# Optimization experiments

Hardware: AMD Instinct MI355X
Metric: run time of the kernel (lower is better)

Reference implementation:

```python
import jax, jax.numpy as jnp
import numpy as np

NUM_HEADS = 16


def setup_inputs() -> dict:
    key = jax.random.key(0)
    ks = jax.random.split(key, 10)
    B, T, D = 2, 2048, 1024
    s = D ** -0.5  # keep activations O(1)
    return {
        "inputs": jax.random.normal(ks[0], (B, T, D), dtype=jnp.float32),
        "mask": jax.random.randint(ks[1], (B, T, T), 0, 2, dtype=jnp.int32),
        "Wq": jax.random.normal(ks[2], (D, D), dtype=jnp.float32) * s,
        "bq": jnp.zeros((D,), dtype=jnp.float32),
        "Wk": jax.random.normal(ks[3], (D, D), dtype=jnp.float32) * s,
        "bk": jnp.zeros((D,), dtype=jnp.float32),
        "Wv": jax.random.normal(ks[4], (D, D), dtype=jnp.float32) * s,
        "bv": jnp.zeros((D,), dtype=jnp.float32),
        "Wo": jax.random.normal(ks[5], (D, D), dtype=jnp.float32) * s,
        "bo": jnp.zeros((D,), dtype=jnp.float32),
    }


def _split_heads(x, h):
    # [B,T,D] -> [B,H,T,D/H]
    B, T, D = x.shape
    return x.reshape(B, T, h, D // h).transpose(0, 2, 1, 3)


def reference(inputs, mask, Wq, bq, Wk, bk, Wv, bv, Wo, bo):
    B, T, D = inputs.shape
    H = NUM_HEADS
    dh = D // H
    q = _split_heads(inputs @ Wq + bq, H) * (dh ** -0.5)  # [B,H,T,dh]
    k = _split_heads(inputs @ Wk + bk, H)
    v = _split_heads(inputs @ Wv + bv, H)
    dot = jnp.einsum("bhqd,bhkd->bhqk", q, k)  # [B,H,T,T]
    m = mask.astype(jnp.float32)[:, None]  # [B,1,T,T]
    dot = dot * m + (1.0 - m) * jnp.finfo(jnp.float32).min
    attn = jax.nn.softmax(dot, axis=-1)
    # dropout inactive at inference (training=False)
    heads = jnp.einsum("bhqk,bhkd->bhqd", attn, v)
    combined = heads.transpose(0, 2, 1, 3).reshape(B, T, D)
    return combined @ Wo + bo
```

## Files before the change

kernel.cpp:

```cpp
#include <hip/hip_runtime.h>
#include <hip/hip_bf16.h>
#include <stdint.h>

typedef _Float16 f16;
typedef __attribute__((ext_vector_type(8))) _Float16 f16x8;
typedef __attribute__((ext_vector_type(2))) __fp16 fp16x2;
typedef __attribute__((ext_vector_type(4))) float f32x4;
typedef __attribute__((ext_vector_type(16))) float f32x16;

#define B_  2
#define T_  2048
#define D_  1024
#define H_  16
#define DH_ 64
#define NSPLIT 2
#define KVSPAN (T_ / NSPLIT)

__device__ __forceinline__ f32x4 mfma16f(f16x8 a, f16x8 b, f32x4 c) {
    return __builtin_amdgcn_mfma_f32_16x16x32_f16(a, b, c, 0, 0, 0);
}
__device__ __forceinline__ f32x16 mfma32f(f16x8 a, f16x8 b, f32x16 c) {
    return __builtin_amdgcn_mfma_f32_32x32x16_f16(a, b, c, 0, 0, 0);
}
__device__ __forceinline__ void gload16(const void* g, void* l) {
    __builtin_amdgcn_global_load_lds(
        (const __attribute__((address_space(1))) uint32_t*)g,
        (__attribute__((address_space(3))) uint32_t*)l, 16, 0, 0);
}
__device__ __forceinline__ float xmax32(float x) {
    float a, b;
    asm("v_mov_b32 %0, %2\n\t"
        "v_mov_b32 %1, %2\n\t"
        "s_nop 1\n\t"
        "v_permlane32_swap_b32 %0, %1\n\t"
        "s_nop 1\n\t"
        "v_max_f32 %0, %0, %1"
        : "=&v"(a), "=&v"(b) : "v"(x));
    return a;
}
__device__ __forceinline__ float xsum32(float x) {
    float a, b;
    asm("v_mov_b32 %0, %2\n\t"
        "v_mov_b32 %1, %2\n\t"
        "s_nop 1\n\t"
        "v_permlane32_swap_b32 %0, %1\n\t"
        "s_nop 1\n\t"
        "v_add_f32 %0, %0, %1"
        : "=&v"(a), "=&v"(b) : "v"(x));
    return a;
}

__global__ __launch_bounds__(256) void maskpack_kernel(
    const int* __restrict__ mask, uint32_t* __restrict__ bitsT)
{
    size_t e = (size_t)blockIdx.x * 256 + threadIdx.x;
    unsigned long long bb = __ballot(mask[e] != 0);
    if ((threadIdx.x & 63) == 0) {
        size_t r = e >> 11;
        int b = (int)(r >> 11), q = (int)(r & (T_ - 1));
        int k = (int)(e & (T_ - 1));
        int w0 = k >> 5;
        size_t base = (size_t)b * (64 * T_) + q;
        bitsT[base + (size_t)w0 * T_]       = (uint32_t)bb;
        bitsT[base + (size_t)(w0 + 1) * T_] = (uint32_t)(bb >> 32);
    }
}

__global__ __launch_bounds__(256) void cvtx_kernel(
    const float* __restrict__ X, f16* __restrict__ Xh)
{
    size_t i0 = ((size_t)blockIdx.x * 256 + threadIdx.x) * 8;
    float4 a = *(const float4*)(X + i0);
    float4 b = *(const float4*)(X + i0 + 4);
    float v[8] = {a.x, a.y, a.z, a.w, b.x, b.y, b.z, b.w};
    f16x8 hh;
#pragma unroll
    for (int i = 0; i < 8; ++i) hh[i] = (f16)v[i];
    *(f16x8*)(Xh + i0) = hh;
}

__global__ __launch_bounds__(256) void wtr_kernel(
    const float* __restrict__ Wq, const float* __restrict__ Wk,
    const float* __restrict__ Wv, const float* __restrict__ Wo,
    f16* __restrict__ WqT, f16* __restrict__ WkT,
    f16* __restrict__ WvT, f16* __restrict__ WoT)
{
    __shared__ float s_t[64][65];
    const int zz = blockIdx.z;
    const float* __restrict__ W = (zz == 0) ? Wq : (zz == 1) ? Wk : (zz == 2) ? Wv : Wo;
    const int k0 = blockIdx.y * 64, n0 = blockIdx.x * 64;
    const int t = threadIdx.x;
    const int r = t >> 2, c0 = (t & 3) * 16;

#pragma unroll
    for (int j = 0; j < 4; ++j) {
        float4 v = *(const float4*)(W + (size_t)(k0 + r) * D_ + n0 + c0 + j * 4);
        s_t[r][c0 + j * 4 + 0] = v.x;
        s_t[r][c0 + j * 4 + 1] = v.y;
        s_t[r][c0 + j * 4 + 2] = v.z;
        s_t[r][c0 + j * 4 + 3] = v.w;
    }
    __syncthreads();

    const int n = t >> 2, kc = (t & 3) * 16;
    f16x8 h0, h1;
#pragma unroll
    for (int j = 0; j < 8; ++j) h0[j] = (f16)s_t[kc + j][n];
#pragma unroll
    for (int j = 0; j < 8; ++j) h1[j] = (f16)s_t[kc + 8 + j][n];
    f16* dh = (zz == 0) ? WqT : (zz == 1) ? WkT : (zz == 2) ? WvT : WoT;
    size_t o = (size_t)(n0 + n) * D_ + k0 + kc;
    *(f16x8*)(dh + o) = h0;
    *(f16x8*)(dh + o + 8) = h1;
}

__global__ __launch_bounds__(256) void gemm_kernel(
    const f16* __restrict__ A, int zbase,
    const f16* __restrict__ BqT, const f16* __restrict__ BkT,
    const f16* __restrict__ BvT, const f16* __restrict__ BoT,
    const float* __restrict__ bq, const float* __restrict__ bk,
    const float* __restrict__ bv, const float* __restrict__ bo,
    f16* __restrict__ Q, f16* __restrict__ K,
    f16* __restrict__ Vt, float* __restrict__ outF)
{
    __shared__ f16 sA[128 * 32];
    __shared__ f16 sB[128 * 32];

    const int z = blockIdx.z + zbase;
    const f16* __restrict__ Bm = (z == 0) ? BqT : (z == 1) ? BkT : (z == 2) ? BvT : BoT;
    const float* __restrict__ bias = (z == 0) ? bq : (z == 1) ? bk : (z == 2) ? bv : bo;

    const int m0 = blockIdx.y * 128;
    const int n0 = blockIdx.x * 128;
    const int tid = threadIdx.x;
    const int w = tid >> 6, l = tid & 63;
    const int g = l >> 4, lr = l & 15;
    const int wm = w >> 1, wn = w & 1;

    const int srow = w * 32 + (l >> 2);
    const int skb  = (l & 3) * 8;

    f32x4 acc[4][4] = {};

    for (int k0 = 0; k0 < D_; k0 += 32) {
        __syncthreads();
#pragma unroll
        for (int i = 0; i < 2; ++i) {
            gload16(A  + (size_t)(m0 + srow + i * 16) * D_ + k0 + skb,
                    &sA[w * 1024 + i * 512]);
            gload16(Bm + (size_t)(n0 + srow + i * 16) * D_ + k0 + skb,
                    &sB[w * 1024 + i * 512]);
        }
        __syncthreads();

        f16x8 ah[4], bh[4];
#pragma unroll
        for (int f = 0; f < 4; ++f) {
            ah[f] = *(const f16x8*)&sA[(wm * 64 + f * 16 + lr) * 32 + g * 8];
            bh[f] = *(const f16x8*)&sB[(wn * 64 + f * 16 + lr) * 32 + g * 8];
        }
#pragma unroll
        for (int fm = 0; fm < 4; ++fm)
#pragma unroll
            for (int fn = 0; fn < 4; ++fn)
                acc[fm][fn] = mfma16f(ah[fm], bh[fn], acc[fm][fn]);
    }

    const float scale = (z == 0) ? 0.125f : 1.0f;
    float biasv[4];
#pragma unroll
    for (int f = 0; f < 4; ++f) biasv[f] = bias[n0 + wn * 64 + f * 16 + lr];

    if (z <= 1) {
        f16* Oq = (z == 0) ? Q : K;
#pragma unroll
        for (int fm = 0; fm < 4; ++fm)
#pragma unroll
            for (int fn = 0; fn < 4; ++fn)
#pragma unroll
                for (int j = 0; j < 4; ++j) {
                    int r = m0 + wm * 64 + fm * 16 + g * 4 + j;
                    int c = n0 + wn * 64 + fn * 16 + lr;
                    float v = (acc[fm][fn][j] + biasv[fn]) * scale;
                    int b = r >> 11, t = r & (T_ - 1);
                    int h = (c >> 6) & 15, d = c & 63;
                    Oq[((size_t)(b * H_ + h) * T_ + t) * DH_ + d] = (f16)v;
                }
    } else if (z == 2) {
#pragma unroll
        for (int fm = 0; fm < 4; ++fm)
#pragma unroll
            for (int fn = 0; fn < 4; ++fn) {
                int r0 = m0 + wm * 64 + fm * 16 + g * 4;
                int c  = n0 + wn * 64 + fn * 16 + lr;
                int b = r0 >> 11, t0 = r0 & (T_ - 1);
                int h = (c >> 6) & 15, d = c & 63;
                union { f16 h4[4]; uint2 u; } pk;
#pragma unroll
                for (int j = 0; j < 4; ++j)
                    pk.h4[j] = (f16)(acc[fm][fn][j] + biasv[fn]);
                *(uint2*)&Vt[(size_t)(b * H_ + h) * (T_ * DH_) +
                             (size_t)(t0 >> 5) * (32 * DH_) + d * 32 + (t0 & 31)] = pk.u;
            }
    } else {
#pragma unroll
        for (int fm = 0; fm < 4; ++fm)
#pragma unroll
            for (int fn = 0; fn < 4; ++fn)
#pragma unroll
                for (int j = 0; j < 4; ++j) {
                    int r = m0 + wm * 64 + fm * 16 + g * 4 + j;
                    int c = n0 + wn * 64 + fn * 16 + lr;
                    outF[(size_t)r * D_ + c] = acc[fm][fn][j] + biasv[fn];
                }
    }
}

__device__ __forceinline__ void attn_tile(
    const f16x8* kh, const f16x8* vb, uint32_t mw, const f16x8* qf,
    f32x16& o0, f32x16& o1, float& m_run, float& l_run)
{
    const float L2E = 1.4426950408889634f;
    f32x16 s = {};
    __builtin_amdgcn_s_setprio(1);
    s = mfma32f(kh[0], qf[0], s);
    s = mfma32f(kh[1], qf[1], s);
    s = mfma32f(kh[2], qf[2], s);
    s = mfma32f(kh[3], qf[3], s);
    __builtin_amdgcn_s_setprio(0);

#pragma unroll
    for (int r = 0; r < 16; ++r) {
        const int bit = (r & 3) + 8 * (r >> 2);
        if (!((mw >> bit) & 1u)) s[r] = -1e30f;
    }

    float t8[8], t4[4];
#pragma unroll
    for (int i = 0; i < 8; ++i) t8[i] = fmaxf(s[i], s[i + 8]);
#pragma unroll
    for (int i = 0; i < 4; ++i) t4[i] = fmaxf(t8[i], t8[i + 4]);
    float pm = fmaxf(fmaxf(t4[0], t4[2]), fmaxf(t4[1], t4[3]));
    pm = xmax32(pm);

    if (__any(pm > m_run + 8.0f)) {
        float mn  = fmaxf(m_run, pm);
        float fac = exp2f((m_run - mn) * L2E);
        l_run *= fac;
#pragma unroll
        for (int r = 0; r < 16; ++r) { o0[r] *= fac; o1[r] *= fac; }
        m_run = mn;
    }

    float p[16];
#pragma unroll
    for (int r = 0; r < 16; ++r) p[r] = exp2f((s[r] - m_run) * L2E);
    float a8[8], a4[4];
#pragma unroll
    for (int i = 0; i < 8; ++i) a8[i] = p[i] + p[i + 8];
#pragma unroll
    for (int i = 0; i < 4; ++i) a4[i] = a8[i] + a8[i + 4];
    float sum = (a4[0] + a4[2]) + (a4[1] + a4[3]);
    sum = xsum32(sum);
    l_run += sum;

    uint32_t wv[8];
#pragma unroll
    for (int m2 = 0; m2 < 8; ++m2) {
        union { fp16x2 h; uint32_t u; } cv;
        cv.h = __builtin_amdgcn_cvt_pkrtz(p[2 * m2], p[2 * m2 + 1]);
        wv[m2] = cv.u;
    }
    asm("v_permlane32_swap_b32 %0, %1" : "+v"(wv[0]), "+v"(wv[2]));
    asm("v_permlane32_swap_b32 %0, %1" : "+v"(wv[1]), "+v"(wv[3]));
    asm("v_permlane32_swap_b32 %0, %1" : "+v"(wv[4]), "+v"(wv[6]));
    asm("v_permlane32_swap_b32 %0, %1" : "+v"(wv[5]), "+v"(wv[7]));
    union { uint32_t u[4]; f16x8 s8; } pa1, pa2;
    pa1.u[0] = wv[0]; pa1.u[1] = wv[1]; pa1.u[2] = wv[2]; pa1.u[3] = wv[3];
    pa2.u[0] = wv[4]; pa2.u[1] = wv[5]; pa2.u[2] = wv[6]; pa2.u[3] = wv[7];

    __builtin_amdgcn_s_setprio(1);
    o0 = mfma32f(vb[0], pa1.s8, o0);
    o0 = mfma32f(vb[1], pa2.s8, o0);
    o1 = mfma32f(vb[2], pa1.s8, o1);
    o1 = mfma32f(vb[3], pa2.s8, o1);
    __builtin_amdgcn_s_setprio(0);
}

__global__ __launch_bounds__(256, 3) void attn_split_kernel(
    const f16* __restrict__ Qg, const f16* __restrict__ Kg,
    const f16* __restrict__ Vt, const uint32_t* __restrict__ bits,
    f16* __restrict__ Op0, f16* __restrict__ Op1,
    float2* __restrict__ stats)
{
    __shared__ f16 sK[2][2048];
    __shared__ f16 sV[2][2048];

    const int bx  = blockIdx.x;
    const int bh  = (bx & 7) | ((bx >> 8) << 3);
    const int mid = (bx >> 3) & 31;
    const int qb  = mid >> 1;
    const int sp  = mid & 1;
    const int b   = bh >> 4, h = bh & 15;
    const int tid = threadIdx.x;
    const int w   = tid >> 6;
    const int l   = tid & 63;
    const int qi  = l & 31;
    const int hl  = l >> 5;
    const int q   = qb * 128 + w * 32 + qi;
    const int kvbase = sp * KVSPAN;

    const size_t hoff = (size_t)(b * H_ + h) * T_ * DH_;
    const f16* Qh = Qg + hoff;
    const f16* Kh = Kg + hoff;
    const f16* Vh = Vt + hoff;
    const uint32_t* mbase = bits + (size_t)b * (64 * T_) + q;

    const int krow = tid >> 3, kch = tid & 7;
    const size_t ksoff = (size_t)krow * DH_ + (size_t)((kch ^ (krow & 7)) * 8);
    const int vrow = tid >> 2, vch = tid & 3;
    const size_t vsoff = (size_t)vrow * 32 + (size_t)((vch ^ ((vrow >> 1) & 3)) * 8);

    f16x8 qf[4];
#pragma unroll
    for (int c = 0; c < 4; ++c)
        qf[c] = *(const f16x8*)&Qh[(size_t)q * DH_ + c * 16 + hl * 8];

    f32x16 o0 = {}; f32x16 o1 = {};
    float m_run = -1e30f, l_run = 0.0f;

#define STAGE(buf, kv)                                                        \
    do {                                                                      \
        gload16(Kh + (size_t)(kv) * DH_ + ksoff, &sK[buf][w * 512]);          \
        gload16(Vh + (size_t)((kv) >> 5) * 2048 + vsoff, &sV[buf][w * 512]);  \
    } while (0)

    STAGE(0, kvbase);
    __syncthreads();

    int cur = 0;
    for (int kv0 = kvbase; kv0 < kvbase + KVSPAN; kv0 += 32) {
        int nxt = kv0 + 32;
        if (nxt == kvbase + KVSPAN) nxt = kvbase;
        STAGE(cur ^ 1, nxt);

        uint32_t mw = mbase[(size_t)(kv0 >> 5) * T_] >> (hl * 4);

        f16x8 kh[4], vb[4];
#pragma unroll
        for (int c = 0; c < 4; ++c)
            kh[c] = *(const f16x8*)&sK[cur][qi * DH_ + (((2 * c + hl) ^ (qi & 7)) << 3)];
#pragma unroll
        for (int j = 0; j < 4; ++j) {
            int row = (j >> 1) * 32 + qi;
            int ch  = ((j & 1) * 2 + hl) ^ ((qi >> 1) & 3);
            vb[j] = *(const f16x8*)&sV[cur][row * 32 + (ch << 3)];
        }

        attn_tile(kh, vb, mw, qf, o0, o1, m_run, l_run);
        __syncthreads();
        cur ^= 1;
    }
#undef STAGE

    float inv = 1.0f / l_run;
    float ov[32];
#pragma unroll
    for (int r = 0; r < 16; ++r) { ov[r] = o0[r]; ov[16 + r] = o1[r]; }
    f16* Op = (sp == 0) ? Op0 : Op1;
    f16* prow = Op + ((size_t)bh * T_ + q) * DH_;
#pragma unroll
    for (int dt = 0; dt < 2; ++dt)
#pragma unroll
        for (int g2 = 0; g2 < 4; ++g2) {
            union { f16 h4[4]; uint2 u; } pk;
#pragma unroll
            for (int j = 0; j < 4; ++j)
                pk.h4[j] = (f16)(ov[dt * 16 + 4 * g2 + j] * inv);
            *(uint2*)(prow + dt * 32 + 8 * g2 + 4 * hl) = pk.u;
        }
    if (hl == 0)
        stats[(size_t)sp * (32 * T_) + (size_t)bh * T_ + q] =
            make_float2(m_run, l_run);
}

__global__ __launch_bounds__(256) void combine_kernel(
    const f16* __restrict__ Op0, const f16* __restrict__ Op1,
    const float2* __restrict__ stats, f16* __restrict__ comb)
{
    const float L2E = 1.4426950408889634f;
    const int row = blockIdx.x * 32 + (threadIdx.x >> 3);
    const int dh0 = (threadIdx.x & 7) * 8;
    const int bh = row >> 11, q = row & (T_ - 1);
    const int b = bh >> 4, h = bh & 15;

    float2 s0 = stats[row];
    float2 s1 = stats[32 * T_ + row];
    float m = fmaxf(s0.x, s1.x);
    float w0 = s0.y * exp2f((s0.x - m) * L2E);
    float w1 = s1.y * exp2f((s1.x - m) * L2E);
    float rs = 1.0f / (w0 + w1);
    float a0 = w0 * rs, a1 = w1 * rs;

    f16x8 v0 = *(const f16x8*)(Op0 + (size_t)row * DH_ + dh0);
    f16x8 v1 = *(const f16x8*)(Op1 + (size_t)row * DH_ + dh0);
    f16x8 ou;
#pragma unroll
    for (int i = 0; i < 8; ++i)
        ou[i] = (f16)(a0 * (float)v0[i] + a1 * (float)v1[i]);
    *(f16x8*)(comb + ((size_t)(b * T_ + q)) * D_ + h * DH_ + dh0) = ou;
}

extern "C" void kernel_launch(void* const* d_in, const int* in_sizes, int n_in,
                              void* d_out, int out_size, void* d_ws, size_t ws_size,
                              hipStream_t stream)
{
    const float* X    = (const float*)d_in[0];
    const int*   mask = (const int*)d_in[1];
    const float* Wq   = (const float*)d_in[2];
    const float* bq   = (const float*)d_in[3];
    const float* Wk   = (const float*)d_in[4];
    const float* bk   = (const float*)d_in[5];
    const float* Wv   = (const float*)d_in[6];
    const float* bv   = (const float*)d_in[7];
    const float* Wo   = (const float*)d_in[8];
    const float* bo   = (const float*)d_in[9];
    float* out = (float*)d_out;

    const size_t SEG  = (size_t)B_ * T_ * D_;
    const size_t WSEG = (size_t)D_ * D_;
    f16* wsp = (f16*)d_ws;
    f16* Q    = wsp + 0 * SEG;
    f16* K    = wsp + 1 * SEG;
    f16* Xh   = wsp + 2 * SEG;
    f16* Op0  = wsp + 3 * SEG;
    f16* WqT  = wsp + 4 * SEG;
    f16* WkT  = WqT + 1 * WSEG;
    f16* WvT  = WqT + 2 * WSEG;
    f16* WoT  = WqT + 3 * WSEG;
    f16* Op1  = wsp + 5 * SEG;
    f16* comb = Xh;
    f16* Vt = (f16*)d_out;
    uint32_t* bits = (uint32_t*)((char*)d_out + (8u << 20));
    float2* stats  = (float2*)((char*)d_out + (9u << 20));

    dim3 blk(256);
    maskpack_kernel<<<dim3((B_ * T_ * T_) / 256), blk, 0, stream>>>(mask, bits);
    cvtx_kernel<<<dim3((B_ * T_ * D_) / 2048), blk, 0, stream>>>(X, Xh);
    wtr_kernel<<<dim3(16, 16, 4), blk, 0, stream>>>(
        Wq, Wk, Wv, Wo, WqT, WkT, WvT, WoT);
    gemm_kernel<<<dim3(D_ / 128, (B_ * T_) / 128, 3), blk, 0, stream>>>(
        Xh, 0, WqT, WkT, WvT, WoT,
        bq, bk, bv, bo, Q, K, Vt, out);
    attn_split_kernel<<<dim3(B_ * H_ * (T_ / 128) * NSPLIT), blk, 0, stream>>>(
        Q, K, Vt, bits, Op0, Op1, stats);
    combine_kernel<<<dim3((32 * T_) / 32), blk, 0, stream>>>(
        Op0, Op1, stats, comb);
    gemm_kernel<<<dim3(D_ / 128, (B_ * T_) / 128, 1), blk, 0, stream>>>(
        comb, 3, WqT, WkT, WvT, WoT,
        bq, bk, bv, bo, Q, K, Vt, out);
}
```

Measured before the change: 161.7 us.

## Widen attention KV tile, add dedicated output-projection GEMM, cheapen softmax reductions

The attention kernel now stages 64 KV rows per iteration as two 32-row halves in shared memory, halving loop iterations and barriers. The output projection moves to its own kernel with a 128x64 tile, doubling its block count for better occupancy on a 256-block grid. Inside the softmax tile, the row-max uses three-input max chains and the row-sum uses packed fp16 dot products against ones. The risks are more shared memory per block and a slightly less precise sum, since it now adds the rounded fp16 probabilities.

New measurement: 161.2 us. Within noise of the previous version (-0.3%).

```diff
diff --git a/kernel.cpp b/kernel.cpp
--- a/kernel.cpp
+++ b/kernel.cpp
@@ -49,6 +49,9 @@
         : "=&v"(a), "=&v"(b) : "v"(x));
     return a;
 }
+__device__ __forceinline__ float max3f(float a, float b, float c) {
+    return fmaxf(fmaxf(a, b), c);
+}
 
 __global__ __launch_bounds__(256) void maskpack_kernel(
     const int* __restrict__ mask, uint32_t* __restrict__ bitsT)
@@ -115,20 +118,19 @@
 }
 
 __global__ __launch_bounds__(256) void gemm_kernel(
-    const f16* __restrict__ A, int zbase,
+    const f16* __restrict__ A,
     const f16* __restrict__ BqT, const f16* __restrict__ BkT,
-    const f16* __restrict__ BvT, const f16* __restrict__ BoT,
+    const f16* __restrict__ BvT,
     const float* __restrict__ bq, const float* __restrict__ bk,
-    const float* __restrict__ bv, const float* __restrict__ bo,
-    f16* __restrict__ Q, f16* __restrict__ K,
-    f16* __restrict__ Vt, float* __restrict__ outF)
+    const float* __restrict__ bv,
+    f16* __restrict__ Q, f16* __restrict__ K, f16* __restrict__ Vt)
 {
     __shared__ f16 sA[128 * 32];
     __shared__ f16 sB[128 * 32];
 
-    const int z = blockIdx.z + zbase;
-    const f16* __restrict__ Bm = (z == 0) ? BqT : (z == 1) ? BkT : (z == 2) ? BvT : BoT;
-    const float* __restrict__ bias = (z == 0) ? bq : (z == 1) ? bk : (z == 2) ? bv : bo;
+    const int z = blockIdx.z;
+    const f16* __restrict__ Bm = (z == 0) ? BqT : (z == 1) ? BkT : BvT;
+    const float* __restrict__ bias = (z == 0) ? bq : (z == 1) ? bk : bv;
 
     const int m0 = blockIdx.y * 128;
     const int n0 = blockIdx.x * 128;
@@ -186,7 +188,7 @@
                     int h = (c >> 6) & 15, d = c & 63;
                     Oq[((size_t)(b * H_ + h) * T_ + t) * DH_ + d] = (f16)v;
                 }
-    } else if (z == 2) {
+    } else {
 #pragma unroll
         for (int fm = 0; fm < 4; ++fm)
 #pragma unroll
@@ -202,18 +204,65 @@
                 *(uint2*)&Vt[(size_t)(b * H_ + h) * (T_ * DH_) +
                              (size_t)(t0 >> 5) * (32 * DH_) + d * 32 + (t0 & 31)] = pk.u;
             }
-    } else {
-#pragma unroll
-        for (int fm = 0; fm < 4; ++fm)
+    }
+}
+
+__global__ __launch_bounds__(256) void oproj_kernel(
+    const f16* __restrict__ A, const f16* __restrict__ BoT,
+    const float* __restrict__ bo, float* __restrict__ outF)
+{
+    __shared__ f16 sA[128 * 32];
+    __shared__ f16 sB[64 * 32];
+
+    const int m0 = blockIdx.y * 128;
+    const int n0 = blockIdx.x * 64;
+    const int tid = threadIdx.x;
+    const int w = tid >> 6, l = tid & 63;
+    const int g = l >> 4, lr = l & 15;
+
+    const int srowA = w * 32 + (l >> 2);
+    const int skbA  = (l & 3) * 8;
+    const int browB = w * 16 + (l >> 2);
+
+    f32x4 acc[2][4] = {};
+
+    for (int k0 = 0; k0 < D_; k0 += 32) {
+        __syncthreads();
+#pragma unroll
+        for (int i = 0; i < 2; ++i)
+            gload16(A + (size_t)(m0 + srowA + i * 16) * D_ + k0 + skbA,
+                    &sA[w * 1024 + i * 512]);
+        gload16(BoT + (size_t)(n0 + browB) * D_ + k0 + skbA,
+                &sB[w * 512]);
+        __syncthreads();
+
+        f16x8 ah[2], bh[4];
+#pragma unroll
+        for (int f = 0; f < 2; ++f)
+            ah[f] = *(const f16x8*)&sA[(w * 32 + f * 16 + lr) * 32 + g * 8];
+#pragma unroll
+        for (int f = 0; f < 4; ++f)
+            bh[f] = *(const f16x8*)&sB[(f * 16 + lr) * 32 + g * 8];
+#pragma unroll
+        for (int fm = 0; fm < 2; ++fm)
 #pragma unroll
             for (int fn = 0; fn < 4; ++fn)
-#pragma unroll
-                for (int j = 0; j < 4; ++j) {
-                    int r = m0 + wm * 64 + fm * 16 + g * 4 + j;
-                    int c = n0 + wn * 64 + fn * 16 + lr;
-                    outF[(size_t)r * D_ + c] = acc[fm][fn][j] + biasv[fn];
-                }
-    }
+                acc[fm][fn] = mfma16f(ah[fm], bh[fn], acc[fm][fn]);
+    }
+
+    float biasv[4];
+#pragma unroll
+    for (int f = 0; f < 4; ++f) biasv[f] = bo[n0 + f * 16 + lr];
+#pragma unroll
+    for (int fm = 0; fm < 2; ++fm)
+#pragma unroll
+        for (int fn = 0; fn < 4; ++fn)
+#pragma unroll
+            for (int j = 0; j < 4; ++j) {
+                int r = m0 + w * 32 + fm * 16 + g * 4 + j;
+                int c = n0 + fn * 16 + lr;
+                outF[(size_t)r * D_ + c] = acc[fm][fn][j] + biasv[fn];
+            }
 }
 
 __device__ __forceinline__ void attn_tile(
@@ -235,12 +284,12 @@
         if (!((mw >> bit) & 1u)) s[r] = -1e30f;
     }
 
-    float t8[8], t4[4];
-#pragma unroll
-    for (int i = 0; i < 8; ++i) t8[i] = fmaxf(s[i], s[i + 8]);
-#pragma unroll
-    for (int i = 0; i < 4; ++i) t4[i] = fmaxf(t8[i], t8[i + 4]);
-    float pm = fmaxf(fmaxf(t4[0], t4[2]), fmaxf(t4[1], t4[3]));
+    float u0 = max3f(s[0],  s[1],  s[2]);
+    float u1 = max3f(s[3],  s[4],  s[5]);
+    float u2 = max3f(s[6],  s[7],  s[8]);
+    float u3 = max3f(s[9],  s[10], s[11]);
+    float u4 = max3f(s[12], s[13], s[14]);
+    float pm = fmaxf(max3f(u0, u1, u2), max3f(u3, u4, s[15]));
     pm = xmax32(pm);
 
     if (__any(pm > m_run + 8.0f)) {
@@ -255,14 +304,6 @@
     float p[16];
 #pragma unroll
     for (int r = 0; r < 16; ++r) p[r] = exp2f((s[r] - m_run) * L2E);
-    float a8[8], a4[4];
-#pragma unroll
-    for (int i = 0; i < 8; ++i) a8[i] = p[i] + p[i + 8];
-#pragma unroll
-    for (int i = 0; i < 4; ++i) a4[i] = a8[i] + a8[i + 4];
-    float sum = (a4[0] + a4[2]) + (a4[1] + a4[3]);
-    sum = xsum32(sum);
-    l_run += sum;
 
     uint32_t wv[8];
 #pragma unroll
@@ -271,6 +312,29 @@
         cv.h = __builtin_amdgcn_cvt_pkrtz(p[2 * m2], p[2 * m2 + 1]);
         wv[m2] = cv.u;
     }
+
+#if __has_builtin(__builtin_amdgcn_fdot2)
+    fp16x2 onep; onep[0] = (__fp16)1.0f; onep[1] = (__fp16)1.0f;
+    float sA_ = 0.0f, sB_ = 0.0f;
+#pragma unroll
+    for (int m2 = 0; m2 < 8; m2 += 2) {
+        union { uint32_t u; fp16x2 h; } ca, cb;
+        ca.u = wv[m2]; cb.u = wv[m2 + 1];
+        sA_ = __builtin_amdgcn_fdot2(ca.h, onep, sA_, false);
+        sB_ = __builtin_amdgcn_fdot2(cb.h, onep, sB_, false);
+    }
+    float sum = sA_ + sB_;
+#else
+    float a8[8], a4[4];
+#pragma unroll
+    for (int i = 0; i < 8; ++i) a8[i] = p[i] + p[i + 8];
+#pragma unroll
+    for (int i = 0; i < 4; ++i) a4[i] = a8[i] + a8[i + 4];
+    float sum = (a4[0] + a4[2]) + (a4[1] + a4[3]);
+#endif
+    sum = xsum32(sum);
+    l_run += sum;
+
     asm("v_permlane32_swap_b32 %0, %1" : "+v"(wv[0]), "+v"(wv[2]));
     asm("v_permlane32_swap_b32 %0, %1" : "+v"(wv[1]), "+v"(wv[3]));
     asm("v_permlane32_swap_b32 %0, %1" : "+v"(wv[4]), "+v"(wv[6]));
@@ -293,8 +357,8 @@
     f16* __restrict__ Op0, f16* __restrict__ Op1,
     float2* __restrict__ stats)
 {
-    __shared__ f16 sK[2][2048];
-    __shared__ f16 sV[2][2048];
+    __shared__ f16 sK[2][64 * 64];
+    __shared__ f16 sV[2][2][64 * 32];
 
     const int bx  = blockIdx.x;
     const int bh  = (bx & 7) | ((bx >> 8) << 3);
@@ -316,10 +380,8 @@
     const f16* Vh = Vt + hoff;
     const uint32_t* mbase = bits + (size_t)b * (64 * T_) + q;
 
-    const int krow = tid >> 3, kch = tid & 7;
-    const size_t ksoff = (size_t)krow * DH_ + (size_t)((kch ^ (krow & 7)) * 8);
-    const int vrow = tid >> 2, vch = tid & 3;
-    const size_t vsoff = (size_t)vrow * 32 + (size_t)((vch ^ ((vrow >> 1) & 3)) * 8);
+    const int krow8 = l >> 3, kch = l & 7;
+    const int vrow16 = l >> 2, vch = l & 3;
 
     f16x8 qf[4];
 #pragma unroll
@@ -329,35 +391,50 @@
     f32x16 o0 = {}; f32x16 o1 = {};
     float m_run = -1e30f, l_run = 0.0f;
 
-#define STAGE(buf, kv)                                                        \
-    do {                                                                      \
-        gload16(Kh + (size_t)(kv) * DH_ + ksoff, &sK[buf][w * 512]);          \
-        gload16(Vh + (size_t)((kv) >> 5) * 2048 + vsoff, &sV[buf][w * 512]);  \
+#define STAGE(buf, kv)                                                         \
+    do {                                                                       \
+        _Pragma("unroll")                                                      \
+        for (int si = 0; si < 2; ++si) {                                       \
+            int krow = si * 32 + w * 8 + krow8;                                \
+            gload16(Kh + (size_t)((kv) + krow) * DH_ +                         \
+                        ((kch ^ (krow & 7)) * 8),                              \
+                    &sK[buf][(size_t)(si * 32 + w * 8) * 64]);                 \
+            int vrow = w * 16 + vrow16;                                        \
+            gload16(Vh + (size_t)(((kv) >> 5) + si) * 2048 + vrow * 32 +       \
+                        ((vch ^ ((vrow >> 1) & 3)) * 8),                       \
+                    &sV[buf][si][(size_t)(w * 16) * 32]);                      \
+        }                                                                      \
     } while (0)
 
     STAGE(0, kvbase);
     __syncthreads();
 
     int cur = 0;
-    for (int kv0 = kvbase; kv0 < kvbase + KVSPAN; kv0 += 32) {
-        int nxt = kv0 + 32;
+    for (int kv0 = kvbase; kv0 < kvbase + KVSPAN; kv0 += 64) {
+        int nxt = kv0 + 64;
         if (nxt == kvbase + KVSPAN) nxt = kvbase;
         STAGE(cur ^ 1, nxt);
 
-        uint32_t mw = mbase[(size_t)(kv0 >> 5) * T_] >> (hl * 4);
-
-        f16x8 kh[4], vb[4];
-#pragma unroll
-        for (int c = 0; c < 4; ++c)
-            kh[c] = *(const f16x8*)&sK[cur][qi * DH_ + (((2 * c + hl) ^ (qi & 7)) << 3)];
-#pragma unroll
-        for (int j = 0; j < 4; ++j) {
-            int row = (j >> 1) * 32 + qi;
-            int ch  = ((j & 1) * 2 + hl) ^ ((qi >> 1) & 3);
-            vb[j] = *(const f16x8*)&sV[cur][row * 32 + (ch << 3)];
+        uint32_t mw0 = mbase[(size_t)(kv0 >> 5) * T_] >> (hl * 4);
+        uint32_t mw1 = mbase[(size_t)((kv0 >> 5) + 1) * T_] >> (hl * 4);
+
+#pragma unroll
+        for (int half = 0; half < 2; ++half) {
+            f16x8 kh[4], vb[4];
+            const int row = qi + 32 * half;
+#pragma unroll
+            for (int c = 0; c < 4; ++c)
+                kh[c] = *(const f16x8*)&sK[cur][row * 64 +
+                            (((2 * c + hl) ^ (row & 7)) << 3)];
+#pragma unroll
+            for (int j = 0; j < 4; ++j) {
+                int vrow = (j >> 1) * 32 + qi;
+                int ch  = ((j & 1) * 2 + hl) ^ ((qi >> 1) & 3);
+                vb[j] = *(const f16x8*)&sV[cur][half][vrow * 32 + (ch << 3)];
+            }
+            attn_tile(kh, vb, half ? mw1 : mw0, qf, o0, o1, m_run, l_run);
         }
 
-        attn_tile(kh, vb, mw, qf, o0, o1, m_run, l_run);
         __syncthreads();
         cur ^= 1;
     }
@@ -450,13 +527,11 @@
     wtr_kernel<<<dim3(16, 16, 4), blk, 0, stream>>>(
         Wq, Wk, Wv, Wo, WqT, WkT, WvT, WoT);
     gemm_kernel<<<dim3(D_ / 128, (B_ * T_) / 128, 3), blk, 0, stream>>>(
-        Xh, 0, WqT, WkT, WvT, WoT,
-        bq, bk, bv, bo, Q, K, Vt, out);
+        Xh, WqT, WkT, WvT, bq, bk, bv, Q, K, Vt);
     attn_split_kernel<<<dim3(B_ * H_ * (T_ / 128) * NSPLIT), blk, 0, stream>>>(
         Q, K, Vt, bits, Op0, Op1, stats);
     combine_kernel<<<dim3((32 * T_) / 32), blk, 0, stream>>>(
         Op0, Op1, stats, comb);
-    gemm_kernel<<<dim3(D_ / 128, (B_ * T_) / 128, 1), blk, 0, stream>>>(
-        comb, 3, WqT, WkT, WvT, WoT,
-        bq, bk, bv, bo, Q, K, Vt, out);
-}
+    oproj_kernel<<<dim3(D_ / 64, (B_ * T_) / 128), blk, 0, stream>>>(
+        comb, WoT, bo, out);
+}
```
